# Kernel optimization log

Measured on AMD Instinct MI355X. Metric: run time of the kernel, lower is better.

## Reference

```python
import jax, jax.numpy as jnp
import numpy as np

HEADS = 16
MAX_SEQ_LEN = 1024
ALPHA = 1.0


def setup_inputs() -> dict:
    key = jax.random.key(0)
    ks = jax.random.split(key, 16)
    b, n, dim = 2, 1024, 1024
    s = 0.02
    x = jax.random.normal(ks[0], (b, n, dim), jnp.float32)
    Wq = jax.random.normal(ks[1], (dim, dim), jnp.float32) * s
    Wk = jax.random.normal(ks[2], (dim, dim), jnp.float32) * s
    Wv = jax.random.normal(ks[3], (dim, dim), jnp.float32) * s
    Wo = jax.random.normal(ks[4], (dim, dim), jnp.float32) * s
    E_idx = jax.random.normal(ks[5], (MAX_SEQ_LEN, HEADS), jnp.float32) * s
    # padding_idx=0 rows zero-initialized (as in torch nn.Embedding(padding_idx=0))
    E_bar = (jax.random.normal(ks[6], (17, HEADS), jnp.float32) * s).at[0].set(0.0)
    E_pos = (jax.random.normal(ks[7], (96, HEADS), jnp.float32) * s).at[0].set(0.0)
    E_oct = (jax.random.normal(ks[8], (25, HEADS), jnp.float32) * s).at[0].set(0.0)
    E_semi = (jax.random.normal(ks[9], (13, HEADS), jnp.float32) * s).at[0].set(0.0)
    # structure matrices: raw values in [0, table_size-2]; forward adds +1
    bar = jax.random.randint(ks[10], (b, n, n), 0, 16, dtype=jnp.int32)
    position = jax.random.randint(ks[11], (b, n, n), 0, 95, dtype=jnp.int32)
    octave = jax.random.randint(ks[12], (b, n, n), 0, 24, dtype=jnp.int32)
    semitone = jax.random.randint(ks[13], (b, n, n), 0, 12, dtype=jnp.int32)
    return {"x": x, "Wq": Wq, "Wk": Wk, "Wv": Wv, "Wo": Wo,
            "E_idx": E_idx, "E_bar": E_bar, "E_pos": E_pos,
            "E_oct": E_oct, "E_semi": E_semi,
            "bar": bar, "position": position, "octave": octave, "semitone": semitone}


def reference(x, Wq, Wk, Wv, Wo, E_idx, E_bar, E_pos, E_oct, E_semi,
              bar, position, octave, semitone):
    b, n, dim = x.shape
    h = HEADS
    d = dim // h

    def split_heads(t):  # (b,n,dim) -> (b,h,n,d)
        return t.reshape(b, n, h, d).transpose(0, 2, 1, 3)

    q = split_heads(x @ Wq.T)
    k = split_heads(x @ Wk.T)
    v = split_heads(x @ Wv.T)

    qk = jnp.einsum('bhid,bhjd->bhij', q, k)

    # relative index bias: (1,h,n,n)
    rel_pos = jnp.clip(jnp.arange(n)[:, None] - jnp.arange(n)[None, :], 0, MAX_SEQ_LEN - 1)
    srel = E_idx[rel_pos].transpose(2, 0, 1)[None]

    # structure biases: embedding lookups -> (b,h,n,n)
    s_time = (E_bar[bar + 1] + E_pos[position + 1]).transpose(0, 3, 1, 2)
    s_pitch = (E_oct[octave + 1] + E_semi[semitone + 1]).transpose(0, 3, 1, 2)

    dots = (qk + ALPHA * (srel + s_time + s_pitch)) / jnp.sqrt(jnp.float32(d))

    causal_mask = jnp.triu(jnp.ones((n, n), dtype=bool), k=1)
    mask_value = -jnp.finfo(dots.dtype).max
    dots = jnp.where(causal_mask, mask_value, dots)

    attn = jax.nn.softmax(dots, axis=-1)  # dropout=0 at eval
    out = jnp.einsum('bhij,bhjd->bhid', attn, v)
    out = out.transpose(0, 2, 1, 3).reshape(b, n, dim)
    return out @ Wo.T
```

## Files before the change

kernel.cpp:

```cpp
#include <hip/hip_runtime.h>
#include <cstdint>
#include <math.h>

typedef __attribute__((ext_vector_type(8))) short short8;
typedef __attribute__((ext_vector_type(4))) float f32x4;

#define LOG2E 1.44269504088896340736f

static __device__ __forceinline__ float bf2f(unsigned short u) {
    union { unsigned int i; float f; } v; v.i = ((unsigned int)u) << 16; return v.f;
}
static __device__ __forceinline__ unsigned short f2bf(float f) {
    union { float f; unsigned int i; } v; v.f = f;
    unsigned int r = v.i + 0x7FFF + ((v.i >> 16) & 1);
    return (unsigned short)(r >> 16);
}

__global__ __launch_bounds__(256) void k_prep(
    const float* __restrict__ x, const float* __restrict__ wq,
    const float* __restrict__ wk, const float* __restrict__ wv,
    const float* __restrict__ wo, unsigned short* __restrict__ dstconv,
    const float* __restrict__ Eidx, const float* __restrict__ Ebar,
    const float* __restrict__ Epos, const float* __restrict__ Eoct,
    const float* __restrict__ Esemi,
    const int* __restrict__ barm, const int* __restrict__ posm,
    const int* __restrict__ octm, const int* __restrict__ semim,
    unsigned short* __restrict__ biasg) {
    __shared__ float2 t2[8 * 233];
    __shared__ int    pk[16 * 65];

    if (blockIdx.x >= 1088) {
        long t = (long)(blockIdx.x - 1088) * 256 + threadIdx.x;
        long base = t * 4;
        const long NX = 2097152, NW = 1048576;
        const float* src; long off;
        if (base < NX)            { src = x;  off = base; }
        else if (base < NX + NW)  { src = wq; off = base - NX; }
        else if (base < NX + 2*NW){ src = wk; off = base - NX - NW; }
        else if (base < NX + 3*NW){ src = wv; off = base - NX - 2*NW; }
        else                      { src = wo; off = base - NX - 3*NW; }
        float4 v = *(const float4*)(src + off);
        ushort4 o;
        o.x = f2bf(v.x); o.y = f2bf(v.y); o.z = f2bf(v.z); o.w = f2bf(v.w);
        *(ushort4*)(dstconv + base) = o;
        return;
    }
    int fid = blockIdx.x;
    int b = (fid >= 544) ? 1 : 0;
    int f = fid - b * 544;
    int ti, tj;
    if (f >= 480) { int rr = f - 480; ti = 60 + (rr >> 4); tj = rr & 15; }
    else {
        int g = (int)(0.5f * (sqrtf(1.0f + 2.0f * (float)f) - 1.0f));
        while (2 * (g + 1) * (g + 2) <= f) g++;
        while (2 * g * (g + 1) > f) g--;
        int rr = f - 2 * g * (g + 1);
        int q = rr / (g + 1);
        ti = g * 4 + q;
        tj = rr - q * (g + 1);
    }
    int i0 = ti * 16, j0 = tj * 64;

    int t = threadIdx.x;
    int rel_lo = i0 - j0 - 63; if (rel_lo < 0) rel_lo = 0;

    for (int idx = t; idx < 231 * 8; idx += 256) {
        int s = idx >> 3, h2 = idx & 7;
        float va, vb;
        if (s < 80) {
            int src = rel_lo + s; if (src > 1023) src = 1023;
            va = Eidx[src * 16 + h2]; vb = Eidx[src * 16 + h2 + 8];
        } else if (s < 97)  { va = Ebar[(s - 80) * 16 + h2];  vb = Ebar[(s - 80) * 16 + h2 + 8]; }
        else if (s < 193)   { va = Epos[(s - 97) * 16 + h2];  vb = Epos[(s - 97) * 16 + h2 + 8]; }
        else if (s < 218)   { va = Eoct[(s - 193) * 16 + h2]; vb = Eoct[(s - 193) * 16 + h2 + 8]; }
        else                { va = Esemi[(s - 218) * 16 + h2]; vb = Esemi[(s - 218) * 16 + h2 + 8]; }
        t2[h2 * 233 + s] = make_float2(va, vb);
    }
    #pragma unroll
    for (int cc = 0; cc < 4; cc++) {
        int cell = t + cc * 256;
        int i = i0 + (cell >> 6), j = j0 + (cell & 63);
        long ij = ((long)b << 20) + ((long)i << 10) + j;
        int v = (barm[ij] + 1) | ((posm[ij] + 1) << 5) |
                ((octm[ij] + 1) << 12) | ((semim[ij] + 1) << 17);
        pk[(cell >> 6) * 65 + (cell & 63)] = v;
    }
    __syncthreads();

    int r = t & 15, h2 = (t >> 4) & 7, ah = t >> 7;
    int i = i0 + r;
    int base_rel = i - j0 - rel_lo;
    const float2* T = &t2[h2 * 233];
    long frag = (r >> 2) * 256 + (r & 3) * 4;
    unsigned short* dstL = biasg + ((((long)(b * 16 + h2)     * 64 + ti) * 16 + tj) << 10) + frag;
    unsigned short* dstH = biasg + ((((long)(b * 16 + h2 + 8) * 64 + ti) * 16 + tj) << 10) + frag;
    #pragma unroll 4
    for (int aa = 0; aa < 8; aa++) {
        int a = ah * 8 + aa;
        ushort4 ovL, ovH;
        #pragma unroll
        for (int jj = 0; jj < 4; jj++) {
            int col = a + 16 * jj;
            int p = pk[r * 65 + col];
            int sr = base_rel - col; if (sr < 0) sr = 0;
            float2 v0 = T[sr];
            float2 v1 = T[80  + (p & 31)];
            float2 v2 = T[97  + ((p >> 5)  & 127)];
            float2 v3 = T[193 + ((p >> 12) & 31)];
            float2 v4 = T[218 + ((p >> 17) & 15)];
            float xL = v0.x + v1.x + v2.x + v3.x + v4.x;
            float xH = v0.y + v1.y + v2.y + v3.y + v4.y;
            ((unsigned short*)&ovL)[jj] = f2bf(xL * 0.125f);
            ((unsigned short*)&ovH)[jj] = f2bf(xH * 0.125f);
        }
        *(ushort4*)(dstL + a * 16) = ovL;
        *(ushort4*)(dstH + a * 16) = ovH;
    }
}

__global__ __launch_bounds__(256) void k_gemm(
    const unsigned short* __restrict__ A,
    const unsigned short* __restrict__ B0, const unsigned short* __restrict__ B1,
    const unsigned short* __restrict__ B2,
    unsigned short* __restrict__ qd, unsigned short* __restrict__ kd,
    unsigned short* __restrict__ vtd, float* __restrict__ outf, int mode) {
    __shared__ unsigned short As[128 * 64];
    __shared__ unsigned short Bs[64 * 64];
    int md = (mode < 0) ? (int)blockIdx.z : mode;
    const unsigned short* B = (md == 1) ? B1 : (md == 2) ? B2 : B0;
    int m0 = blockIdx.x * 128, n0 = blockIdx.y * 64;
    int t = threadIdx.x;
    int w = t >> 6, lane = t & 63, g = lane >> 4, c = lane & 15;
    int wr = w >> 1, wc = w & 1;
    const int K = 1024;
    f32x4 zero = {0.f, 0.f, 0.f, 0.f};
    f32x4 acc[4][2];
    #pragma unroll
    for (int m = 0; m < 4; m++)
        #pragma unroll
        for (int n = 0; n < 2; n++) acc[m][n] = zero;

    int srow = w * 8 + (lane >> 3);
    int scol = (lane & 7) * 8;
    for (int k0 = 0; k0 < K; k0 += 64) {
        __syncthreads();
        #pragma unroll
        for (int q = 0; q < 4; q++) {
            int row = q * 32 + srow;
            __builtin_amdgcn_global_load_lds(
                (const __attribute__((address_space(1))) unsigned int*)(A + (long)(m0 + row) * K + k0 + scol),
                (__attribute__((address_space(3))) unsigned int*)&As[(q * 32 + w * 8) * 64],
                16, 0, 0);
        }
        #pragma unroll
        for (int q = 0; q < 2; q++) {
            int row = q * 32 + srow;
            __builtin_amdgcn_global_load_lds(
                (const __attribute__((address_space(1))) unsigned int*)(B + (long)(n0 + row) * K + k0 + scol),
                (__attribute__((address_space(3))) unsigned int*)&Bs[(q * 32 + w * 8) * 64],
                16, 0, 0);
        }
        __syncthreads();
        #pragma unroll
        for (int kk = 0; kk < 2; kk++) {
            short8 a[4], bb[2];
            #pragma unroll
            for (int m = 0; m < 4; m++)
                a[m] = *(const short8*)&As[(wr * 64 + m * 16 + c) * 64 + kk * 32 + g * 8];
            #pragma unroll
            for (int n = 0; n < 2; n++)
                bb[n] = *(const short8*)&Bs[(wc * 32 + n * 16 + c) * 64 + kk * 32 + g * 8];
            #pragma unroll
            for (int m = 0; m < 4; m++)
                #pragma unroll
                for (int n = 0; n < 2; n++)
                    acc[m][n] = __builtin_amdgcn_mfma_f32_16x16x32_bf16(a[m], bb[n], acc[m][n], 0, 0, 0);
        }
    }

    if (md <= 1) {
        unsigned short* dst = (md == 0) ? qd : kd;
        float scale = (md == 0) ? 0.125f : 1.0f;
        #pragma unroll
        for (int m = 0; m < 4; m++) {
            #pragma unroll
            for (int r = 0; r < 4; r++) {
                int mm = m0 + wr * 64 + m * 16 + g * 4 + r;
                int bb2 = mm >> 10, ii = mm & 1023;
                #pragma unroll
                for (int n = 0; n < 2; n++) {
                    int nn = n0 + wc * 32 + n * 16 + c;
                    int hh = nn >> 6, dd = nn & 63;
                    dst[(((long)(bb2 * 16 + hh) << 10) + ii) * 64 + dd] = f2bf(acc[m][n][r] * scale);
                }
            }
        }
    } else if (md == 2) {
        #pragma unroll
        for (int m = 0; m < 4; m++) {
            int mm0 = m0 + wr * 64 + m * 16 + g * 4;
            int bb2 = mm0 >> 10, ii = mm0 & 1023;
            #pragma unroll
            for (int n = 0; n < 2; n++) {
                int nn = n0 + wc * 32 + n * 16 + c;
                int hh = nn >> 6, dd = nn & 63;
                ushort4 pkv;
                pkv.x = f2bf(acc[m][n][0]); pkv.y = f2bf(acc[m][n][1]);
                pkv.z = f2bf(acc[m][n][2]); pkv.w = f2bf(acc[m][n][3]);
                *(ushort4*)&vtd[(((long)(bb2 * 16 + hh) << 6) + dd) * 1024 + ii] = pkv;
            }
        }
    } else {
        #pragma unroll
        for (int m = 0; m < 4; m++) {
            #pragma unroll
            for (int r = 0; r < 4; r++) {
                long mm = m0 + wr * 64 + m * 16 + g * 4 + r;
                #pragma unroll
                for (int n = 0; n < 2; n++) {
                    int nn = n0 + wc * 32 + n * 16 + c;
                    outf[mm * 1024 + nn] = acc[m][n][r];
                }
            }
        }
    }
}

#define LOADT(KA, KB, BV, JT) do {                                             \
    int _j0 = (JT) * 64;                                                       \
    _Pragma("unroll")                                                          \
    for (int _s = 0; _s < 4; _s++) {                                           \
        const unsigned short* _kr = Kp + (long)(_j0 + _s * 16 + c) * 64 + g * 8; \
        KA[_s] = *(const short8*)(_kr);                                        \
        KB[_s] = *(const short8*)(_kr + 32);                                   \
    }                                                                          \
    const unsigned short* _bp = Bt + ((JT) << 10) + lane * 16;                 \
    BV[0] = *(const short8*)(_bp);                                             \
    BV[1] = *(const short8*)(_bp + 8);                                         \
} while (0)

#define BODY(KA, KB, BV, JT, POFS) do {                                        \
    int _j0 = (JT) * 64;                                                       \
    f32x4 _s[4];                                                               \
    _Pragma("unroll")                                                          \
    for (int _jj = 0; _jj < 4; _jj++) {                                        \
        _s[_jj] = __builtin_amdgcn_mfma_f32_16x16x32_bf16(q0, KA[_jj], zero, 0, 0, 0); \
        _s[_jj] = __builtin_amdgcn_mfma_f32_16x16x32_bf16(q1, KB[_jj], _s[_jj], 0, 0, 0); \
    }                                                                          \
    short8 _v0[4], _v1[4];                                                     \
    _Pragma("unroll")                                                          \
    for (int _dd = 0; _dd < 4; _dd++) {                                        \
        const unsigned short* _vb = Vp + (long)(_dd * 16 + c) * 1024 + _j0 + g * 8; \
        _v0[_dd] = *(const short8*)(_vb);                                      \
        _v1[_dd] = *(const short8*)(_vb + 32);                                 \
    }                                                                          \
    _Pragma("unroll")                                                          \
    for (int _r = 0; _r < 4; _r++) {                                           \
        _Pragma("unroll")                                                      \
        for (int _jj = 0; _jj < 4; _jj++) {                                    \
            int _idx = _r * 4 + _jj;                                           \
            float _bb = (_idx < 8) ? bf2f((unsigned short)BV[0][_idx])         \
                                   : bf2f((unsigned short)BV[1][_idx - 8]);    \
            _s[_jj][_r] += _bb;                                                \
        }                                                                      \
    }                                                                          \
    if ((JT) == nj - 1) {                                                      \
        _Pragma("unroll")                                                      \
        for (int _r = 0; _r < 4; _r++) {                                       \
            int _i = i0 + g * 4 + _r;                                          \
            _Pragma("unroll")                                                  \
            for (int _jj = 0; _jj < 4; _jj++)                                  \
                if (_j0 + _jj * 16 + c > _i) _s[_jj][_r] = -1e9f;              \
        }                                                                      \
    }                                                                          \
    unsigned short* _p = (unsigned short*)(wbase + (POFS));                    \
    _Pragma("unroll")                                                          \
    for (int _r = 0; _r < 4; _r++) {                                           \
        _Pragma("unroll")                                                      \
        for (int _jj = 0; _jj < 4; _jj++) {                                    \
            float _pv = exp2f(__builtin_fmaf(_s[_jj][_r], LOG2E, -8.0f * LOG2E)); \
            l[_r] += _pv;                                                      \
            union { float f; unsigned int u; } _pu; _pu.f = _pv;               \
            _p[(g * 4 + _r) * 72 + c + 16 * _jj] = (unsigned short)(_pu.u >> 16); \
        }                                                                      \
    }                                                                          \
    short8 _pa0 = *(const short8*)&_p[c * 72 + g * 8];                         \
    short8 _pa1 = *(const short8*)&_p[c * 72 + 32 + g * 8];                    \
    _Pragma("unroll")                                                          \
    for (int _dd = 0; _dd < 4; _dd++) {                                        \
        o[_dd] = __builtin_amdgcn_mfma_f32_16x16x32_bf16(_pa0, _v0[_dd], o[_dd], 0, 0, 0); \
        o[_dd] = __builtin_amdgcn_mfma_f32_16x16x32_bf16(_pa1, _v1[_dd], o[_dd], 0, 0, 0); \
    }                                                                          \
} while (0)

__global__ __launch_bounds__(256) void k_attn(
    const unsigned short* __restrict__ Qs, const unsigned short* __restrict__ Ks,
    const unsigned short* __restrict__ VTs, const unsigned short* __restrict__ biasg,
    unsigned short* __restrict__ Os) {
    __shared__ char smem[4 * 5632];
    int bid = blockIdx.x;
    int it = 63 - (bid >> 5);
    int bh = bid & 31;
    int b = bh >> 4, h = bh & 15;
    int w = threadIdx.x >> 6;
    int lane = threadIdx.x & 63;
    int g = lane >> 4, c = lane & 15;
    int i0 = it * 16;

    char* wbase = smem + w * 5632;

    long plane = ((long)bh) << 16;
    const unsigned short* Qp = Qs + plane;
    const unsigned short* Kp = Ks + plane;
    const unsigned short* Vp = VTs + plane;
    const unsigned short* Bt = biasg + (((long)bh * 64 + it) << 14);

    short8 q0 = *(const short8*)(Qp + (long)(i0 + c) * 64 + g * 8);
    short8 q1 = *(const short8*)(Qp + (long)(i0 + c) * 64 + 32 + g * 8);

    f32x4 zero = {0.f, 0.f, 0.f, 0.f};
    f32x4 o[4]; o[0] = zero; o[1] = zero; o[2] = zero; o[3] = zero;
    float l[4] = {0.f, 0.f, 0.f, 0.f};

    int nj = (it >> 2) + 1;
    short8 kaA[4], kbA[4], bvA[2];
    short8 kaB[4], kbB[4], bvB[2];
    if (w < nj) LOADT(kaA, kbA, bvA, w);
    for (int jt = w; jt < nj; jt += 8) {
        if (jt + 4 < nj) LOADT(kaB, kbB, bvB, jt + 4);
        BODY(kaA, kbA, bvA, jt, 0);
        if (jt + 4 < nj) {
            if (jt + 8 < nj) LOADT(kaA, kbA, bvA, jt + 8);
            BODY(kaB, kbB, bvB, jt + 4, 2304);
        }
    }
    float* oc = (float*)wbase;
    float* lc = (float*)(wbase + 4352);
    #pragma unroll
    for (int dd = 0; dd < 4; dd++)
        #pragma unroll
        for (int r = 0; r < 4; r++)
            oc[lane * 17 + dd * 4 + r] = o[dd][r];
    #pragma unroll
    for (int r = 0; r < 4; r++) lc[lane * 5 + r] = l[r];
    __syncthreads();

    {
        int r = w;
        float lv = 0.f;
        #pragma unroll
        for (int ww = 0; ww < 4; ww++)
            lv += ((const float*)(smem + ww * 5632 + 4352))[lane * 5 + r];
        lv += __shfl_xor(lv, 1); lv += __shfl_xor(lv, 2);
        lv += __shfl_xor(lv, 4); lv += __shfl_xor(lv, 8);
        float linv = 1.0f / lv;
        int i = i0 + g * 4 + r;
        unsigned short* op = Os + ((long)(b * 1024 + i)) * 1024 + h * 64;
        #pragma unroll
        for (int dd = 0; dd < 4; dd++) {
            float ov = 0.f;
            #pragma unroll
            for (int ww = 0; ww < 4; ww++)
                ov += ((const float*)(smem + ww * 5632))[lane * 17 + dd * 4 + r];
            op[dd * 16 + c] = f2bf(ov * linv);
        }
    }
}

extern "C" void kernel_launch(void* const* d_in, const int* in_sizes, int n_in,
                              void* d_out, int out_size, void* d_ws, size_t ws_size,
                              hipStream_t stream) {
    const float* x     = (const float*)d_in[0];
    const float* Wq    = (const float*)d_in[1];
    const float* Wk    = (const float*)d_in[2];
    const float* Wv    = (const float*)d_in[3];
    const float* Wo    = (const float*)d_in[4];
    const float* Eidx  = (const float*)d_in[5];
    const float* Ebar  = (const float*)d_in[6];
    const float* Epos  = (const float*)d_in[7];
    const float* Eoct  = (const float*)d_in[8];
    const float* Esemi = (const float*)d_in[9];
    const int* barm    = (const int*)d_in[10];
    const int* posm    = (const int*)d_in[11];
    const int* octm    = (const int*)d_in[12];
    const int* semim   = (const int*)d_in[13];
    float* outf = (float*)d_out;

    unsigned short* w = (unsigned short*)d_ws;
    unsigned short* XB   = w;
    unsigned short* WQB  = w + 2097152;
    unsigned short* WKB  = w + 3145728;
    unsigned short* WVB  = w + 4194304;
    unsigned short* WOB  = w + 5242880;
    unsigned short* QS   = w + 6291456;
    unsigned short* KS   = w + 8388608;
    unsigned short* VTS  = w + 10485760;
    unsigned short* OS   = w + 12582912;
    unsigned short* BIAS = w + 14680064;

    k_prep<<<7232, 256, 0, stream>>>(x, Wq, Wk, Wv, Wo, w,
                                     Eidx, Ebar, Epos, Eoct, Esemi,
                                     barm, posm, octm, semim, BIAS);
    k_gemm<<<dim3(16, 16, 3), 256, 0, stream>>>(XB, WQB, WKB, WVB,
                                                QS, KS, VTS, nullptr, -1);
    k_attn<<<2048, 256, 0, stream>>>(QS, KS, VTS, BIAS, OS);
    k_gemm<<<dim3(16, 16, 1), 256, 0, stream>>>(OS, WOB, WOB, WOB,
                                                QS, KS, VTS, outf, 3);
}
```

Baseline: 105.3 us.

## Compute transposed S in attention, pass P via lane shuffles instead of LDS

The attention body swaps the MFMA operands so each lane holds scores for one query across keys. The probabilities are packed to bf16 with v_cvt_pk_bf16_f32 and redistributed through __shfl into the B operand of the PV MFMA, so P no longer round-trips through per-wave LDS. The bias precompute kernel is rewritten to emit the matching transposed bias fragment layout, with each thread producing four heads. The output epilogue is changed to vectorized ushort4 stores. This trades LDS writes/reads and the implicit wait for extra cross-lane shuffles and select operations.

```diff
diff --git a/kernel.cpp b/kernel.cpp
--- a/kernel.cpp
+++ b/kernel.cpp
@@ -87,34 +87,42 @@
     }
     __syncthreads();
 
-    int r = t & 15, h2 = (t >> 4) & 7, ah = t >> 7;
-    int i = i0 + r;
-    int base_rel = i - j0 - rel_lo;
-    const float2* T = &t2[h2 * 233];
-    long frag = (r >> 2) * 256 + (r & 3) * 4;
-    unsigned short* dstL = biasg + ((((long)(b * 16 + h2)     * 64 + ti) * 16 + tj) << 10) + frag;
-    unsigned short* dstH = biasg + ((((long)(b * 16 + h2 + 8) * 64 + ti) * 16 + tj) << 10) + frag;
-    #pragma unroll 4
-    for (int aa = 0; aa < 8; aa++) {
-        int a = ah * 8 + aa;
-        ushort4 ovL, ovH;
-        #pragma unroll
-        for (int jj = 0; jj < 4; jj++) {
-            int col = a + 16 * jj;
-            int p = pk[r * 65 + col];
-            int sr = base_rel - col; if (sr < 0) sr = 0;
-            float2 v0 = T[sr];
-            float2 v1 = T[80  + (p & 31)];
-            float2 v2 = T[97  + ((p >> 5)  & 127)];
-            float2 v3 = T[193 + ((p >> 12) & 31)];
-            float2 v4 = T[218 + ((p >> 17) & 15)];
-            float xL = v0.x + v1.x + v2.x + v3.x + v4.x;
-            float xH = v0.y + v1.y + v2.y + v3.y + v4.y;
-            ((unsigned short*)&ovL)[jj] = f2bf(xL * 0.125f);
-            ((unsigned short*)&ovH)[jj] = f2bf(xH * 0.125f);
-        }
-        *(ushort4*)(dstL + a * 16) = ovL;
-        *(ushort4*)(dstH + a * 16) = ovH;
+    int lane = t & 63, q = t & 15, G = (t >> 4) & 3, hq = t >> 6;
+    int base_rel = (i0 + q) - j0 - rel_lo;
+    const float2* TA = &t2[hq * 233];
+    const float2* TB = &t2[(hq + 4) * 233];
+    long tbase = ((((long)(b * 16) * 64 + ti) * 16 + tj) << 10) + lane * 16;
+    #pragma unroll
+    for (int sub = 0; sub < 4; sub++) {
+        ushort4 o0, o1, o2, o3;
+        #pragma unroll
+        for (int rr = 0; rr < 4; rr++) {
+            int key = sub * 16 + G * 4 + rr;
+            int p = pk[q * 65 + key];
+            int sr = base_rel - key; if (sr < 0) sr = 0;
+            float2 a0 = TA[sr];
+            float2 a1 = TA[80  + (p & 31)];
+            float2 a2 = TA[97  + ((p >> 5)  & 127)];
+            float2 a3 = TA[193 + ((p >> 12) & 31)];
+            float2 a4 = TA[218 + ((p >> 17) & 15)];
+            float2 b0 = TB[sr];
+            float2 b1 = TB[80  + (p & 31)];
+            float2 b2 = TB[97  + ((p >> 5)  & 127)];
+            float2 b3 = TB[193 + ((p >> 12) & 31)];
+            float2 b4 = TB[218 + ((p >> 17) & 15)];
+            float xA = a0.x + a1.x + a2.x + a3.x + a4.x;
+            float yA = a0.y + a1.y + a2.y + a3.y + a4.y;
+            float xB = b0.x + b1.x + b2.x + b3.x + b4.x;
+            float yB = b0.y + b1.y + b2.y + b3.y + b4.y;
+            ((unsigned short*)&o0)[rr] = f2bf(xA * 0.125f);
+            ((unsigned short*)&o1)[rr] = f2bf(xB * 0.125f);
+            ((unsigned short*)&o2)[rr] = f2bf(yA * 0.125f);
+            ((unsigned short*)&o3)[rr] = f2bf(yB * 0.125f);
+        }
+        *(ushort4*)(biasg + tbase + ((long)hq        << 20) + sub * 4) = o0;
+        *(ushort4*)(biasg + tbase + ((long)(hq + 4)  << 20) + sub * 4) = o1;
+        *(ushort4*)(biasg + tbase + ((long)(hq + 8)  << 20) + sub * 4) = o2;
+        *(ushort4*)(biasg + tbase + ((long)(hq + 12) << 20) + sub * 4) = o3;
     }
 }
 
@@ -145,19 +153,19 @@
     for (int k0 = 0; k0 < K; k0 += 64) {
         __syncthreads();
         #pragma unroll
-        for (int q = 0; q < 4; q++) {
-            int row = q * 32 + srow;
+        for (int qq = 0; qq < 4; qq++) {
+            int row = qq * 32 + srow;
             __builtin_amdgcn_global_load_lds(
                 (const __attribute__((address_space(1))) unsigned int*)(A + (long)(m0 + row) * K + k0 + scol),
-                (__attribute__((address_space(3))) unsigned int*)&As[(q * 32 + w * 8) * 64],
+                (__attribute__((address_space(3))) unsigned int*)&As[(qq * 32 + w * 8) * 64],
                 16, 0, 0);
         }
         #pragma unroll
-        for (int q = 0; q < 2; q++) {
-            int row = q * 32 + srow;
+        for (int qq = 0; qq < 2; qq++) {
+            int row = qq * 32 + srow;
             __builtin_amdgcn_global_load_lds(
                 (const __attribute__((address_space(1))) unsigned int*)(B + (long)(n0 + row) * K + k0 + scol),
-                (__attribute__((address_space(3))) unsigned int*)&Bs[(q * 32 + w * 8) * 64],
+                (__attribute__((address_space(3))) unsigned int*)&Bs[(qq * 32 + w * 8) * 64],
                 16, 0, 0);
         }
         __syncthreads();
@@ -239,65 +247,66 @@
     BV[1] = *(const short8*)(_bp + 8);                                         \
 } while (0)
 
-#define BODY(KA, KB, BV, JT, POFS) do {                                        \
-    int _j0 = (JT) * 64;                                                       \
-    f32x4 _s[4];                                                               \
-    _Pragma("unroll")                                                          \
-    for (int _jj = 0; _jj < 4; _jj++) {                                        \
-        _s[_jj] = __builtin_amdgcn_mfma_f32_16x16x32_bf16(q0, KA[_jj], zero, 0, 0, 0); \
-        _s[_jj] = __builtin_amdgcn_mfma_f32_16x16x32_bf16(q1, KB[_jj], _s[_jj], 0, 0, 0); \
-    }                                                                          \
-    short8 _v0[4], _v1[4];                                                     \
-    _Pragma("unroll")                                                          \
-    for (int _dd = 0; _dd < 4; _dd++) {                                        \
+#define BODY(KA, KB, BV, JT) do {                                             \
+    int _j0 = (JT) * 64;                                                      \
+    f32x4 _s[4];                                                              \
+    _Pragma("unroll")                                                         \
+    for (int _sub = 0; _sub < 4; _sub++) {                                    \
+        _s[_sub] = __builtin_amdgcn_mfma_f32_16x16x32_bf16(KA[_sub], q0, zero, 0, 0, 0); \
+        _s[_sub] = __builtin_amdgcn_mfma_f32_16x16x32_bf16(KB[_sub], q1, _s[_sub], 0, 0, 0); \
+    }                                                                         \
+    short8 _v0[4], _v1[4];                                                    \
+    _Pragma("unroll")                                                         \
+    for (int _dd = 0; _dd < 4; _dd++) {                                       \
         const unsigned short* _vb = Vp + (long)(_dd * 16 + c) * 1024 + _j0 + g * 8; \
-        _v0[_dd] = *(const short8*)(_vb);                                      \
-        _v1[_dd] = *(const short8*)(_vb + 32);                                 \
-    }                                                                          \
-    _Pragma("unroll")                                                          \
-    for (int _r = 0; _r < 4; _r++) {                                           \
-        _Pragma("unroll")                                                      \
-        for (int _jj = 0; _jj < 4; _jj++) {                                    \
-            int _idx = _r * 4 + _jj;                                           \
-            float _bb = (_idx < 8) ? bf2f((unsigned short)BV[0][_idx])         \
-                                   : bf2f((unsigned short)BV[1][_idx - 8]);    \
-            _s[_jj][_r] += _bb;                                                \
-        }                                                                      \
-    }                                                                          \
-    if ((JT) == nj - 1) {                                                      \
-        _Pragma("unroll")                                                      \
-        for (int _r = 0; _r < 4; _r++) {                                       \
-            int _i = i0 + g * 4 + _r;                                          \
-            _Pragma("unroll")                                                  \
-            for (int _jj = 0; _jj < 4; _jj++)                                  \
-                if (_j0 + _jj * 16 + c > _i) _s[_jj][_r] = -1e9f;              \
-        }                                                                      \
-    }                                                                          \
-    unsigned short* _p = (unsigned short*)(wbase + (POFS));                    \
-    _Pragma("unroll")                                                          \
-    for (int _r = 0; _r < 4; _r++) {                                           \
-        _Pragma("unroll")                                                      \
-        for (int _jj = 0; _jj < 4; _jj++) {                                    \
-            float _pv = exp2f(__builtin_fmaf(_s[_jj][_r], LOG2E, -8.0f * LOG2E)); \
-            l[_r] += _pv;                                                      \
-            union { float f; unsigned int u; } _pu; _pu.f = _pv;               \
-            _p[(g * 4 + _r) * 72 + c + 16 * _jj] = (unsigned short)(_pu.u >> 16); \
-        }                                                                      \
-    }                                                                          \
-    short8 _pa0 = *(const short8*)&_p[c * 72 + g * 8];                         \
-    short8 _pa1 = *(const short8*)&_p[c * 72 + 32 + g * 8];                    \
-    _Pragma("unroll")                                                          \
-    for (int _dd = 0; _dd < 4; _dd++) {                                        \
-        o[_dd] = __builtin_amdgcn_mfma_f32_16x16x32_bf16(_pa0, _v0[_dd], o[_dd], 0, 0, 0); \
-        o[_dd] = __builtin_amdgcn_mfma_f32_16x16x32_bf16(_pa1, _v1[_dd], o[_dd], 0, 0, 0); \
-    }                                                                          \
+        _v0[_dd] = *(const short8*)(_vb);                                     \
+        _v1[_dd] = *(const short8*)(_vb + 32);                                \
+    }                                                                         \
+    unsigned int _P0[4], _P1[4];                                              \
+    _Pragma("unroll")                                                         \
+    for (int _sub = 0; _sub < 4; _sub++) {                                    \
+        float _pe[4];                                                         \
+        _Pragma("unroll")                                                     \
+        for (int _r = 0; _r < 4; _r++) {                                      \
+            int _idx = _sub * 4 + _r;                                         \
+            float _ss = _s[_sub][_r] +                                        \
+                ((_idx < 8) ? bf2f((unsigned short)BV[0][_idx])               \
+                            : bf2f((unsigned short)BV[1][_idx - 8]));         \
+            if ((JT) == nj - 1 && _j0 + _sub * 16 + g * 4 + _r > i0 + c)      \
+                _ss = -1e9f;                                                  \
+            _pe[_r] = exp2f(__builtin_fmaf(_ss, LOG2E, -8.0f * LOG2E));       \
+            l += _pe[_r];                                                     \
+        }                                                                     \
+        asm("v_cvt_pk_bf16_f32 %0, %1, %2" : "=v"(_P0[_sub]) : "v"(_pe[0]), "v"(_pe[1])); \
+        asm("v_cvt_pk_bf16_f32 %0, %1, %2" : "=v"(_P1[_sub]) : "v"(_pe[2]), "v"(_pe[3])); \
+    }                                                                         \
+    _Pragma("unroll")                                                         \
+    for (int _ch = 0; _ch < 2; _ch++) {                                       \
+        unsigned int _a0 = (unsigned int)__shfl((int)_P0[_ch * 2],     srcA); \
+        unsigned int _a1 = (unsigned int)__shfl((int)_P0[_ch * 2 + 1], srcA); \
+        unsigned int _b0 = (unsigned int)__shfl((int)_P1[_ch * 2],     srcA); \
+        unsigned int _b1 = (unsigned int)__shfl((int)_P1[_ch * 2 + 1], srcA); \
+        unsigned int _c0 = (unsigned int)__shfl((int)_P0[_ch * 2],     srcB); \
+        unsigned int _c1 = (unsigned int)__shfl((int)_P0[_ch * 2 + 1], srcB); \
+        unsigned int _d0 = (unsigned int)__shfl((int)_P1[_ch * 2],     srcB); \
+        unsigned int _d1 = (unsigned int)__shfl((int)_P1[_ch * 2 + 1], srcB); \
+        union { unsigned int u[4]; short8 s8; } _pb;                          \
+        _pb.u[0] = sel ? _a1 : _a0;                                           \
+        _pb.u[1] = sel ? _b1 : _b0;                                           \
+        _pb.u[2] = sel ? _c1 : _c0;                                           \
+        _pb.u[3] = sel ? _d1 : _d0;                                           \
+        _Pragma("unroll")                                                     \
+        for (int _dd = 0; _dd < 4; _dd++)                                     \
+            o[_dd] = __builtin_amdgcn_mfma_f32_16x16x32_bf16(                 \
+                (_ch == 0) ? _v0[_dd] : _v1[_dd], _pb.s8, o[_dd], 0, 0, 0);   \
+    }                                                                         \
 } while (0)
 
 __global__ __launch_bounds__(256) void k_attn(
     const unsigned short* __restrict__ Qs, const unsigned short* __restrict__ Ks,
     const unsigned short* __restrict__ VTs, const unsigned short* __restrict__ biasg,
     unsigned short* __restrict__ Os) {
-    __shared__ char smem[4 * 5632];
+    __shared__ char smem[4 * 4672];
     int bid = blockIdx.x;
     int it = 63 - (bid >> 5);
     int bh = bid & 31;
@@ -306,8 +315,11 @@
     int lane = threadIdx.x & 63;
     int g = lane >> 4, c = lane & 15;
     int i0 = it * 16;
-
-    char* wbase = smem + w * 5632;
+    int srcA = ((lane >> 4) & 1) * 32 + c;
+    int srcB = srcA + 16;
+    int sel  = (lane >> 5) & 1;
+
+    char* wbase = smem + w * 4672;
 
     long plane = ((long)bh) << 16;
     const unsigned short* Qp = Qs + plane;
@@ -320,7 +332,7 @@
 
     f32x4 zero = {0.f, 0.f, 0.f, 0.f};
     f32x4 o[4]; o[0] = zero; o[1] = zero; o[2] = zero; o[3] = zero;
-    float l[4] = {0.f, 0.f, 0.f, 0.f};
+    float l = 0.f;
 
     int nj = (it >> 2) + 1;
     short8 kaA[4], kbA[4], bvA[2];
@@ -328,42 +340,46 @@
     if (w < nj) LOADT(kaA, kbA, bvA, w);
     for (int jt = w; jt < nj; jt += 8) {
         if (jt + 4 < nj) LOADT(kaB, kbB, bvB, jt + 4);
-        BODY(kaA, kbA, bvA, jt, 0);
+        BODY(kaA, kbA, bvA, jt);
         if (jt + 4 < nj) {
             if (jt + 8 < nj) LOADT(kaA, kbA, bvA, jt + 8);
-            BODY(kaB, kbB, bvB, jt + 4, 2304);
+            BODY(kaB, kbB, bvB, jt + 4);
         }
     }
     float* oc = (float*)wbase;
     float* lc = (float*)(wbase + 4352);
     #pragma unroll
-    for (int dd = 0; dd < 4; dd++)
+    for (int db = 0; db < 4; db++)
         #pragma unroll
         for (int r = 0; r < 4; r++)
-            oc[lane * 17 + dd * 4 + r] = o[dd][r];
-    #pragma unroll
-    for (int r = 0; r < 4; r++) lc[lane * 5 + r] = l[r];
+            oc[lane * 17 + db * 4 + r] = o[db][r];
+    lc[lane] = l;
     __syncthreads();
 
     {
-        int r = w;
+        int db = w;
         float lv = 0.f;
         #pragma unroll
         for (int ww = 0; ww < 4; ww++)
-            lv += ((const float*)(smem + ww * 5632 + 4352))[lane * 5 + r];
-        lv += __shfl_xor(lv, 1); lv += __shfl_xor(lv, 2);
-        lv += __shfl_xor(lv, 4); lv += __shfl_xor(lv, 8);
+            lv += ((const float*)(smem + ww * 4672 + 4352))[lane];
+        lv += __shfl_xor(lv, 16);
+        lv += __shfl_xor(lv, 32);
         float linv = 1.0f / lv;
-        int i = i0 + g * 4 + r;
-        unsigned short* op = Os + ((long)(b * 1024 + i)) * 1024 + h * 64;
-        #pragma unroll
-        for (int dd = 0; dd < 4; dd++) {
-            float ov = 0.f;
+        float ov[4];
+        #pragma unroll
+        for (int r = 0; r < 4; r++) {
+            float s = 0.f;
             #pragma unroll
             for (int ww = 0; ww < 4; ww++)
-                ov += ((const float*)(smem + ww * 5632))[lane * 17 + dd * 4 + r];
-            op[dd * 16 + c] = f2bf(ov * linv);
-        }
+                s += ((const float*)(smem + ww * 4672))[lane * 17 + db * 4 + r];
+            ov[r] = s;
+        }
+        int i = i0 + c;
+        unsigned short* op = Os + ((long)(b * 1024 + i)) * 1024 + h * 64 + db * 16 + g * 4;
+        ushort4 o4;
+        o4.x = f2bf(ov[0] * linv); o4.y = f2bf(ov[1] * linv);
+        o4.z = f2bf(ov[2] * linv); o4.w = f2bf(ov[3] * linv);
+        *(ushort4*)op = o4;
     }
 }
 
```

Measured after the change: 103.5 us, median of 2. About the same (-1.7%).
